# Optimization experiments

Measured on AMD Instinct MI355X. Metric: run time of the kernel, lower is better.

The kernel has to match this reference:

```python
import jax, jax.numpy as jnp
import numpy as np

B, T = 256, 512
E, H, V, C = 128, 256, 50000, 64


def setup_inputs() -> dict:
    key = jax.random.key(0)
    ks = jax.random.split(key, 8)
    k = 1.0 / np.sqrt(H)
    u = lambda kk, shape: jax.random.uniform(kk, shape, jnp.float32, -k, k)
    return {
        "sentence": jax.random.randint(ks[0], (B, T), 0, V),
        "emb": jax.random.normal(ks[1], (V, E), jnp.float32),
        "W_ih": u(ks[2], (4 * H, E)),
        "W_hh": u(ks[3], (4 * H, H)),
        "b_ih": u(ks[4], (4 * H,)),
        "b_hh": u(ks[5], (4 * H,)),
        "W_lin": u(ks[6], (C, H)),
        "b_lin": u(ks[7], (C,)),
    }


def reference(sentence, emb, W_ih, W_hh, b_ih, b_hh, W_lin, b_lin):
    x = emb[sentence]  # [B, T, E]
    # Precompute input-to-gate projections for all timesteps in one GEMM.
    x_proj = jnp.einsum('bte,ge->btg', x, W_ih) + b_ih + b_hh  # [B, T, 4H]

    def step(carry, xt):
        h, c = carry
        gates = xt + h @ W_hh.T  # [B, 4H], torch gate order i,f,g,o
        i, f, g, o = jnp.split(gates, 4, axis=-1)
        c = jax.nn.sigmoid(f) * c + jax.nn.sigmoid(i) * jnp.tanh(g)
        h = jax.nn.sigmoid(o) * jnp.tanh(c)
        return (h, c), h

    h0 = jnp.zeros((x.shape[0], W_hh.shape[1]), x.dtype)
    _, hs = jax.lax.scan(step, (h0, h0), jnp.swapaxes(x_proj, 0, 1))
    lstm_out = jnp.swapaxes(hs, 0, 1)  # [B, T, H]

    logits = lstm_out @ W_lin.T + b_lin  # [B, T, C]
    # Faithful to original: LogSoftmax over dim=1 (the TIME axis), then prod over time.
    all_probs = jax.nn.log_softmax(logits, axis=1)
    return jnp.prod(all_probs, axis=1)  # [B, C]
```

## Files before the change

kernel.cpp:

```cpp
#include <hip/hip_runtime.h>

#define TT 512
#define HH 256
#define EE 128
#define BB 256
#define CC 64
#define VV 50000
#define NSB 128

#define OFF_EMB   0ull
#define OFF_WHA   6400000ull
#define OFF_WXA   6662144ull
#define OFF_BIAS  6793216ull
#define OFF_WLIN  6797312ull
#define OFF_LSTM  6813696ull
#define OFF_LOG   73922560ull
#define WS_NEED   107476992ull

typedef __attribute__((ext_vector_type(4))) float    f32x4;
typedef __attribute__((ext_vector_type(4))) unsigned u32x4;
typedef __attribute__((ext_vector_type(4))) int      i32x4;
typedef __attribute__((ext_vector_type(8))) int      i32x8;
typedef __bf16 bf16x8_t __attribute__((ext_vector_type(8)));

__device__ __forceinline__ float rcp_f(float x) { return __builtin_amdgcn_rcpf(x); }
__device__ __forceinline__ float exp2_(float x) {
  float r; asm("v_exp_f32 %0, %1" : "=v"(r) : "v"(x)); return r;
}
__device__ __forceinline__ unsigned short to_bf16(float f) {
  unsigned u = __float_as_uint(f);
  return (unsigned short)((u + 0x7fffu + ((u >> 16) & 1u)) >> 16);
}
__device__ __forceinline__ unsigned enc4(float v) {
  const unsigned sg = (__float_as_uint(v) >> 31) << 3;
  const float a = fminf(fabsf(v), 6.0f);
  const float c = (a < 2.0f) ? __builtin_rintf(a + a)
                : (a < 4.0f) ? __builtin_rintf(a) + 2.0f
                             : __builtin_rintf(a * 0.5f) + 4.0f;
  return sg | (unsigned)(int)c;
}
__device__ __forceinline__ i32x8 up8(i32x4 v) {
  i32x8 r;
  r[0] = v[0]; r[1] = v[1]; r[2] = v[2]; r[3] = v[3];
  r[4] = 0; r[5] = 0; r[6] = 0; r[7] = 0;
  return r;
}
__device__ __forceinline__ f32x4 mfma4(i32x8 a, i32x8 b, f32x4 c, int sb) {
  return __builtin_amdgcn_mfma_scale_f32_16x16x128_f8f6f4(
      a, b, c, 4, 4, 0, 0x7f7f7f7f, 0, sb);
}
#define SB_H 0x7f7f7f7f
#define SB_X 0x80808080

#define LOG2E  1.442695041f
#define SN2    (-LOG2E / 256.f)
#define SG2    (-2.f * LOG2E / 256.f)
#define C2_    (-2.f * LOG2E)

__global__ void prep_emb(const float* __restrict__ emb, unsigned* __restrict__ out) {
  const int u = blockIdx.x * 256 + threadIdx.x;
  const f32x4 f0 = ((const f32x4*)emb)[u * 2];
  const f32x4 f1 = ((const f32x4*)emb)[u * 2 + 1];
  unsigned r = enc4(2.f * f0[0]) | (enc4(2.f * f0[1]) << 4);
  r |= (enc4(2.f * f0[2]) | (enc4(2.f * f0[3]) << 4)) << 8;
  r |= (enc4(2.f * f1[0]) | (enc4(2.f * f1[1]) << 4)) << 16;
  r |= (enc4(2.f * f1[2]) | (enc4(2.f * f1[3]) << 4)) << 24;
  out[u] = r;
}

__global__ void prep_wha(const float* __restrict__ Whh, unsigned char* __restrict__ wf) {
  const int id = blockIdx.x * 256 + threadIdx.x;
  const int byt = id & 15, l = (id >> 4) & 63;
  const int kt = (id >> 10) & 1, mt = (id >> 11) & 7, w8 = id >> 14;
  const int r16 = l & 15;
  const int grow = (r16 & 3) * 256 + w8 * 32 + mt * 4 + (r16 >> 2);
  const int k0 = kt * 128 + ((l >> 4) << 5) + byt * 2;
  const unsigned n0 = enc4(64.f * Whh[grow * HH + k0]);
  const unsigned n1 = enc4(64.f * Whh[grow * HH + k0 + 1]);
  wf[id] = (unsigned char)(n0 | (n1 << 4));
}

__global__ void prep_wxa(const float* __restrict__ Wih, unsigned char* __restrict__ wf) {
  const int id = blockIdx.x * 256 + threadIdx.x;
  const int byt = id & 15, l = (id >> 4) & 63;
  const int mt = (id >> 10) & 7, w8 = id >> 13;
  const int r16 = l & 15;
  const int grow = (r16 & 3) * 256 + w8 * 32 + mt * 4 + (r16 >> 2);
  const int k0 = ((l >> 4) << 5) + byt * 2;
  const unsigned n0 = enc4(64.f * Wih[grow * EE + k0]);
  const unsigned n1 = enc4(64.f * Wih[grow * EE + k0 + 1]);
  wf[id] = (unsigned char)(n0 | (n1 << 4));
}

__global__ void prep_bias(const float* __restrict__ bih, const float* __restrict__ bhh,
                          float* __restrict__ bp) {
  const int n = blockIdx.x * 256 + threadIdx.x;
  const float sc = (n >= 512 && n < 768) ? (-2.f * LOG2E) : (-LOG2E);
  bp[n] = (bih[n] + bhh[n]) * sc;
}

__global__ void prep_wlin(const float* __restrict__ Wlin, unsigned short* __restrict__ wl) {
  const int id = blockIdx.x * 256 + threadIdx.x;
  const int j = id & 7, l = (id >> 3) & 63;
  const int kk = (id >> 9) & 7, q = id >> 12;
  const int c = q * 16 + (l & 15);
  const int k = kk * 32 + ((l >> 4) << 3) + j;
  wl[id] = to_bf16(Wlin[c * HH + k]);
}

__global__ __launch_bounds__(1024, 1)
void lstm_scan(const int* __restrict__ sent, const unsigned char* __restrict__ emb4,
               const unsigned char* __restrict__ wha, const unsigned char* __restrict__ wxa,
               const float* __restrict__ bias, unsigned short* __restrict__ lstm_out) {
  __shared__ __align__(16) unsigned char xa[64 * 1024];
  __shared__ __align__(16) unsigned char bh[2 * 1024];
  __shared__ __align__(16) unsigned char xbuf[2][1024];
  __shared__ __align__(16) float redistf[16][272];
  __shared__ int sent_lds[4][512];

  const int tid = threadIdx.x;
  const int lane = tid & 63;
  const int w = tid >> 6;
  const int b0 = blockIdx.x << 2;

  i32x8 Ah[4][2];
#pragma unroll
  for (int m = 0; m < 4; ++m)
#pragma unroll
    for (int kt = 0; kt < 2; ++kt)
      Ah[m][kt] = up8(*(const i32x4*)(wha + (((w * 4 + m) * 2 + kt) * 64 + lane) * 16));

  for (int c = tid; c < 4096; c += 1024)
    ((u32x4*)xa)[c] = ((const u32x4*)wxa)[c];
  for (int i = tid; i < 2048; i += 1024)
    sent_lds[i >> 9][i & 511] = sent[(b0 + (i >> 9)) * TT + (i & 511)];
  if (tid < 512) ((int*)bh)[tid] = 0;

  const bool gth = (w < 8) && (lane < 8);
  const int gr = 2 * w + ((lane >> 2) & 1), gq = lane & 3;
  const int* sptr = &sent_lds[gr & 3][gr >> 2];
  const unsigned char* embg = emb4 + gq * 16;
  const int gwo = gq * 256 + gr * 16;

  __syncthreads();

  u32x4 xg;
  if (gth) {
    const int i0s = sptr[0];
    *(u32x4*)(xbuf[0] + gwo) = *(const u32x4*)(embg + (size_t)i0s * 64);
    const int i1s = sptr[4];
    *(u32x4*)(xbuf[1] + gwo) = *(const u32x4*)(embg + (size_t)i1s * 64);
    const int i2s = sptr[8];
    xg = *(const u32x4*)(embg + (size_t)i2s * 64);
  }
  __syncthreads();

  const int l16 = lane * 16;
  const f32x4 Zf = (f32x4){0.f, 0.f, 0.f, 0.f};
  f32x4 acc[4];
  {
    const i32x8 Bx = up8(*(const i32x4*)(xbuf[0] + l16));
#pragma unroll
    for (int m = 0; m < 4; ++m)
      acc[m] = mfma4(up8(*(const i32x4*)(xa + (w * 4 + m) * 1024 + l16)), Bx, Zf, SB_X);
  }

  const int s = lane & 3;
  const int hu = w * 16 + (lane >> 2);
  const int colJ = (lane & 15) >> 2;
  const float bi = bias[hu],       bf = bias[256 + hu],
              bg = bias[512 + hu], bo = bias[768 + hu];
  const int cb4 = (hu >> 7) * 1024 + ((hu & 127) >> 5) * 256 + s * 16 + ((hu & 31) >> 1);
  const int wroff = (lane >> 4) * 16 + s * 4;
  const int rdoff = (lane >> 4) * 68 + ((lane >> 2) & 3) * 16 + s * 4;
  const bool heven = ((lane >> 2) & 1) == 0;
  const long obase = ((long)(b0 + s) * TT) * HH + hu;
  float cs = 0.f;

#define MICRO(J) { \
  const i32x8 Bh0 = up8(*(const i32x4*)(bh + l16)); \
  const i32x8 Bh1 = up8(*(const i32x4*)(bh + 1024 + l16)); \
  __builtin_amdgcn_s_setprio(1); \
  _Pragma("unroll") for (int m = 0; m < 4; ++m) acc[m] = mfma4(Ah[m][0], Bh0, acc[m], SB_H); \
  _Pragma("unroll") for (int m = 0; m < 4; ++m) acc[m] = mfma4(Ah[m][1], Bh1, acc[m], SB_H); \
  __builtin_amdgcn_s_setprio(0); \
  if (colJ == (J)) { \
    _Pragma("unroll") for (int m = 0; m < 4; ++m) \
      *(f32x4*)&redistf[w][m * 68 + wroff] = acc[m]; \
  } \
  if ((J) == 2) { \
    if (dogS) *(u32x4*)(xbC + gwo) = xg; \
    if (dogL) { const int idx = sptr[(tb + 3) * 4]; \
                xg = *(const u32x4*)(embg + (size_t)idx * 64); } \
  } \
  if ((J) == 3) { \
    const i32x8 Bx = up8(*(const i32x4*)(xbN + l16)); \
    _Pragma("unroll") for (int m = 0; m < 4; ++m) \
      acc[m] = mfma4(up8(*(const i32x4*)(xa + (w * 4 + m) * 1024 + l16)), Bx, Zf, SB_X); \
  } \
  asm volatile("s_waitcnt lgkmcnt(0)" ::: "memory"); \
  __builtin_amdgcn_sched_barrier(0); \
  const f32x4 g = *(const f32x4*)&redistf[w][rdoff]; \
  const float si = rcp_f(1.f + exp2_(g[0] * SN2 + bi)); \
  const float sf = rcp_f(1.f + exp2_(g[1] * SN2 + bf)); \
  const float tg = 2.f * rcp_f(1.f + exp2_(g[2] * SG2 + bg)) - 1.f; \
  const float so = rcp_f(1.f + exp2_(g[3] * SN2 + bo)); \
  cs = sf * cs + si * tg; \
  const float tc = 2.f * rcp_f(1.f + exp2_(cs * C2_)) - 1.f; \
  const float hv = so * tc; \
  const float hvp = __shfl_xor(hv, 4); \
  if (heven) { \
    const unsigned nib = enc4(4.f * hv) | (enc4(4.f * hvp) << 4); \
    bh[cb4 + ((((J) + 1) & 3)) * 64] = (unsigned char)nib; \
    bh[cb4 + (J) * 64] = 0; \
    unsigned pb; asm("v_cvt_pk_bf16_f32 %0, %1, %2" : "=v"(pb) : "v"(hv), "v"(hvp)); \
    *(unsigned*)(lstm_out + obase + (long)(t0 + (J)) * HH) = pb; \
  } \
  asm volatile("s_waitcnt lgkmcnt(0)" ::: "memory"); \
  __builtin_amdgcn_s_barrier(); \
}

#pragma unroll 1
  for (int tb = 0; tb < NSB; ++tb) {
    const int t0 = tb << 2;
    const bool dogS = gth && (tb + 2 < NSB);
    const bool dogL = gth && (tb + 3 < NSB);
    unsigned char* xbC = xbuf[tb & 1];
    unsigned char* xbN = xbuf[(tb + 1) & 1];
    MICRO(0)
    MICRO(1)
    MICRO(2)
    MICRO(3)
  }
#undef MICRO
}

__global__ __launch_bounds__(256)
void logits_gemm(const unsigned short* __restrict__ lstm, const unsigned short* __restrict__ wl,
                 const float* __restrict__ blin, float* __restrict__ logits) {
  const int tid = threadIdx.x, l = tid & 63, wv = tid >> 6;
  const long m0 = (long)blockIdx.x * 64 + wv * 16;
  f32x4 ac[4];
#pragma unroll
  for (int q = 0; q < 4; ++q) ac[q] = (f32x4){0.f, 0.f, 0.f, 0.f};
  const unsigned short* arow = lstm + (m0 + (l & 15)) * HH + ((l >> 4) << 3);
#pragma unroll
  for (int kk = 0; kk < 8; ++kk) {
    const bf16x8_t a = __builtin_bit_cast(bf16x8_t, *(const u32x4*)(arow + kk * 32));
#pragma unroll
    for (int q = 0; q < 4; ++q) {
      const bf16x8_t b = __builtin_bit_cast(bf16x8_t, *(const u32x4*)(wl + (((q * 8 + kk) * 64 + l) << 3)));
      ac[q] = __builtin_amdgcn_mfma_f32_16x16x32_bf16(a, b, ac[q], 0, 0, 0);
    }
  }
  const int r0 = (l >> 4) << 2;
#pragma unroll
  for (int q = 0; q < 4; ++q) {
    const int col = q * 16 + (l & 15);
    const float bb = blin[col];
#pragma unroll
    for (int r = 0; r < 4; ++r)
      logits[(m0 + r0 + r) * CC + col] = ac[q][r] + bb;
  }
}

__global__ __launch_bounds__(256)
void softmax_prod(const float* __restrict__ logits, float* __restrict__ out) {
  __shared__ float lds[TT * CC];
  __shared__ float red[3][4][CC];
  const int tid = threadIdx.x, b = blockIdx.x;
  const f32x4* src = (const f32x4*)(logits + (long)b * TT * CC);
  f32x4* dst = (f32x4*)lds;
#pragma unroll 1
  for (int i = tid; i < TT * CC / 4; i += 256) dst[i] = src[i];
  __syncthreads();

  const int c = tid & 63, part = tid >> 6;
  const int t0 = part * 128;
  float m = -3.0e38f;
  for (int k = 0; k < 128; ++k) m = fmaxf(m, lds[(t0 + k) * CC + c]);
  red[0][part][c] = m;
  __syncthreads();
  m = fmaxf(fmaxf(red[0][0][c], red[0][1][c]), fmaxf(red[0][2][c], red[0][3][c]));

  float ssum = 0.f;
  for (int k = 0; k < 128; ++k) ssum += __expf(lds[(t0 + k) * CC + c] - m);
  red[1][part][c] = ssum;
  __syncthreads();
  ssum = red[1][0][c] + red[1][1][c] + red[1][2][c] + red[1][3][c];
  const float lse = m + __logf(ssum);

  float pacc = 0.f;
  for (int k = 0; k < 128; ++k) pacc += __log2f(fabsf(lds[(t0 + k) * CC + c] - lse));
  red[2][part][c] = pacc;
  __syncthreads();
  if (part == 0) {
    const float tot = red[2][0][c] + red[2][1][c] + red[2][2][c] + red[2][3][c];
    out[b * CC + c] = exp2f(fminf(tot, 127.0f));
  }
}

extern "C" void kernel_launch(void* const* d_in, const int* in_sizes, int n_in,
                              void* d_out, int out_size, void* d_ws, size_t ws_size,
                              hipStream_t stream) {
  (void)in_sizes; (void)n_in; (void)out_size;
  if (ws_size < WS_NEED) return;

  const int*   sent = (const int*)d_in[0];
  const float* emb  = (const float*)d_in[1];
  const float* Wih  = (const float*)d_in[2];
  const float* Whh  = (const float*)d_in[3];
  const float* bih  = (const float*)d_in[4];
  const float* bhh  = (const float*)d_in[5];
  const float* Wlin = (const float*)d_in[6];
  const float* blin = (const float*)d_in[7];
  float* out = (float*)d_out;
  char* ws = (char*)d_ws;

  unsigned char*  emb4 = (unsigned char*)(ws + OFF_EMB);
  unsigned char*  wha  = (unsigned char*)(ws + OFF_WHA);
  unsigned char*  wxa  = (unsigned char*)(ws + OFF_WXA);
  float*          bp   = (float*)(ws + OFF_BIAS);
  unsigned short* wl   = (unsigned short*)(ws + OFF_WLIN);
  unsigned short* lo   = (unsigned short*)(ws + OFF_LSTM);
  float*          lg   = (float*)(ws + OFF_LOG);

  prep_emb<<<3125, 256, 0, stream>>>(emb, (unsigned*)emb4);
  prep_wha<<<512, 256, 0, stream>>>(Whh, wha);
  prep_wxa<<<256, 256, 0, stream>>>(Wih, wxa);
  prep_bias<<<4, 256, 0, stream>>>(bih, bhh, bp);
  prep_wlin<<<64, 256, 0, stream>>>(Wlin, wl);
  lstm_scan<<<64, 1024, 0, stream>>>(sent, emb4, wha, wxa, bp, lo);
  logits_gemm<<<2048, 256, 0, stream>>>(lo, wl, blin, lg);
  softmax_prod<<<256, 256, 0, stream>>>(lg, out);
}
```

Baseline: 564.6 us.

## Split LSTM scan into 2-batch blocks of 8 waves with fused gate reciprocals

The recurrent scan kernel now gives each workgroup 2 batch rows instead of 4. It launches 128 blocks of 512 threads instead of 64 blocks of 1024, so more CUs take part in the serial scan. Each wave now owns 32 hidden units (8 MFMA tiles), and the time loop unrolls 8 steps per block iteration, with the redistribution and embedding-prefetch indexing remapped to match. The gate math also merges reciprocals: pairs of sigmoid and tanh denominators are multiplied together so each step needs 3 rcp instead of 6. This trades a shorter dependent chain and more parallel blocks for more register pressure per wave and a small risk of overflow in the combined denominators.

After: 514.7 us. 8.8% less time.

```diff
diff --git a/kernel.cpp b/kernel.cpp
--- a/kernel.cpp
+++ b/kernel.cpp
@@ -6,7 +6,7 @@
 #define BB 256
 #define CC 64
 #define VV 50000
-#define NSB 128
+#define NSB 64
 
 #define OFF_EMB   0ull
 #define OFF_WHA   6400000ull
@@ -108,37 +108,37 @@
   wl[id] = to_bf16(Wlin[c * HH + k]);
 }
 
-__global__ __launch_bounds__(1024, 1)
+__global__ __launch_bounds__(512, 1)
 void lstm_scan(const int* __restrict__ sent, const unsigned char* __restrict__ emb4,
                const unsigned char* __restrict__ wha, const unsigned char* __restrict__ wxa,
                const float* __restrict__ bias, unsigned short* __restrict__ lstm_out) {
   __shared__ __align__(16) unsigned char xa[64 * 1024];
   __shared__ __align__(16) unsigned char bh[2 * 1024];
   __shared__ __align__(16) unsigned char xbuf[2][1024];
-  __shared__ __align__(16) float redistf[16][272];
-  __shared__ int sent_lds[4][512];
+  __shared__ __align__(16) float redistf[8][544];
+  __shared__ int sent_lds[2][512];
 
   const int tid = threadIdx.x;
   const int lane = tid & 63;
   const int w = tid >> 6;
-  const int b0 = blockIdx.x << 2;
-
-  i32x8 Ah[4][2];
-#pragma unroll
-  for (int m = 0; m < 4; ++m)
+  const int b0 = blockIdx.x << 1;
+
+  i32x8 Ah[8][2];
+#pragma unroll
+  for (int mt = 0; mt < 8; ++mt)
 #pragma unroll
     for (int kt = 0; kt < 2; ++kt)
-      Ah[m][kt] = up8(*(const i32x4*)(wha + (((w * 4 + m) * 2 + kt) * 64 + lane) * 16));
-
-  for (int c = tid; c < 4096; c += 1024)
+      Ah[mt][kt] = up8(*(const i32x4*)(wha + (((w * 8 + mt) * 2 + kt) * 64 + lane) * 16));
+
+  for (int c = tid; c < 4096; c += 512)
     ((u32x4*)xa)[c] = ((const u32x4*)wxa)[c];
-  for (int i = tid; i < 2048; i += 1024)
+  for (int i = tid; i < 1024; i += 512)
     sent_lds[i >> 9][i & 511] = sent[(b0 + (i >> 9)) * TT + (i & 511)];
   if (tid < 512) ((int*)bh)[tid] = 0;
 
-  const bool gth = (w < 8) && (lane < 8);
+  const bool gth = lane < 8;
   const int gr = 2 * w + ((lane >> 2) & 1), gq = lane & 3;
-  const int* sptr = &sent_lds[gr & 3][gr >> 2];
+  const int* sptr = &sent_lds[gr & 1][gr >> 1];
   const unsigned char* embg = emb4 + gq * 16;
   const int gwo = gq * 256 + gr * 16;
 
@@ -148,32 +148,35 @@
   if (gth) {
     const int i0s = sptr[0];
     *(u32x4*)(xbuf[0] + gwo) = *(const u32x4*)(embg + (size_t)i0s * 64);
-    const int i1s = sptr[4];
+    const int i1s = sptr[8];
     *(u32x4*)(xbuf[1] + gwo) = *(const u32x4*)(embg + (size_t)i1s * 64);
-    const int i2s = sptr[8];
+    const int i2s = sptr[16];
     xg = *(const u32x4*)(embg + (size_t)i2s * 64);
   }
   __syncthreads();
 
   const int l16 = lane * 16;
   const f32x4 Zf = (f32x4){0.f, 0.f, 0.f, 0.f};
-  f32x4 acc[4];
+  f32x4 acc[8];
   {
     const i32x8 Bx = up8(*(const i32x4*)(xbuf[0] + l16));
 #pragma unroll
-    for (int m = 0; m < 4; ++m)
-      acc[m] = mfma4(up8(*(const i32x4*)(xa + (w * 4 + m) * 1024 + l16)), Bx, Zf, SB_X);
-  }
-
-  const int s = lane & 3;
-  const int hu = w * 16 + (lane >> 2);
-  const int colJ = (lane & 15) >> 2;
+    for (int mt = 0; mt < 8; ++mt)
+      acc[mt] = mfma4(up8(*(const i32x4*)(xa + ((w * 8 + mt) << 10) + l16)), Bx, Zf, SB_X);
+  }
+
+  const int s = lane & 1;
+  const int huL = lane >> 1;
+  const int hu = w * 32 + huL;
+  const int mtR = lane >> 3;
+  const int hulR = (lane >> 1) & 3;
   const float bi = bias[hu],       bf = bias[256 + hu],
               bg = bias[512 + hu], bo = bias[768 + hu];
-  const int cb4 = (hu >> 7) * 1024 + ((hu & 127) >> 5) * 256 + s * 16 + ((hu & 31) >> 1);
+  const int wc = (lane & 15) >> 1;
   const int wroff = (lane >> 4) * 16 + s * 4;
-  const int rdoff = (lane >> 4) * 68 + ((lane >> 2) & 3) * 16 + s * 4;
-  const bool heven = ((lane >> 2) & 1) == 0;
+  const int rdoff = mtR * 68 + hulR * 16 + s * 4;
+  const bool heven = (huL & 1) == 0;
+  const int cb4s = (hu >> 7) * 1024 + ((hu & 127) >> 5) * 256 + ((hu & 31) >> 1) + s * 16;
   const long obase = ((long)(b0 + s) * TT) * HH + hu;
   float cs = 0.f;
 
@@ -181,40 +184,43 @@
   const i32x8 Bh0 = up8(*(const i32x4*)(bh + l16)); \
   const i32x8 Bh1 = up8(*(const i32x4*)(bh + 1024 + l16)); \
   __builtin_amdgcn_s_setprio(1); \
-  _Pragma("unroll") for (int m = 0; m < 4; ++m) acc[m] = mfma4(Ah[m][0], Bh0, acc[m], SB_H); \
-  _Pragma("unroll") for (int m = 0; m < 4; ++m) acc[m] = mfma4(Ah[m][1], Bh1, acc[m], SB_H); \
+  _Pragma("unroll") for (int mt = 0; mt < 8; ++mt) acc[mt] = mfma4(Ah[mt][0], Bh0, acc[mt], SB_H); \
+  _Pragma("unroll") for (int mt = 0; mt < 8; ++mt) acc[mt] = mfma4(Ah[mt][1], Bh1, acc[mt], SB_H); \
   __builtin_amdgcn_s_setprio(0); \
-  if (colJ == (J)) { \
-    _Pragma("unroll") for (int m = 0; m < 4; ++m) \
-      *(f32x4*)&redistf[w][m * 68 + wroff] = acc[m]; \
+  if (wc == (J)) { \
+    _Pragma("unroll") for (int mt = 0; mt < 8; ++mt) \
+      *(f32x4*)&redistf[w][mt * 68 + wroff] = acc[mt]; \
   } \
-  if ((J) == 2) { \
+  if ((J) == 4) { \
     if (dogS) *(u32x4*)(xbC + gwo) = xg; \
-    if (dogL) { const int idx = sptr[(tb + 3) * 4]; \
+    if (dogL) { const int idx = sptr[(tb + 3) * 8]; \
                 xg = *(const u32x4*)(embg + (size_t)idx * 64); } \
   } \
-  if ((J) == 3) { \
+  if ((J) == 7) { \
     const i32x8 Bx = up8(*(const i32x4*)(xbN + l16)); \
-    _Pragma("unroll") for (int m = 0; m < 4; ++m) \
-      acc[m] = mfma4(up8(*(const i32x4*)(xa + (w * 4 + m) * 1024 + l16)), Bx, Zf, SB_X); \
+    _Pragma("unroll") for (int mt = 0; mt < 8; ++mt) \
+      acc[mt] = mfma4(up8(*(const i32x4*)(xa + ((w * 8 + mt) << 10) + l16)), Bx, Zf, SB_X); \
   } \
   asm volatile("s_waitcnt lgkmcnt(0)" ::: "memory"); \
   __builtin_amdgcn_sched_barrier(0); \
   const f32x4 g = *(const f32x4*)&redistf[w][rdoff]; \
-  const float si = rcp_f(1.f + exp2_(g[0] * SN2 + bi)); \
-  const float sf = rcp_f(1.f + exp2_(g[1] * SN2 + bf)); \
-  const float tg = 2.f * rcp_f(1.f + exp2_(g[2] * SG2 + bg)) - 1.f; \
-  const float so = rcp_f(1.f + exp2_(g[3] * SN2 + bo)); \
-  cs = sf * cs + si * tg; \
-  const float tc = 2.f * rcp_f(1.f + exp2_(cs * C2_)) - 1.f; \
-  const float hv = so * tc; \
-  const float hvp = __shfl_xor(hv, 4); \
+  const float ea = exp2_(g[0] * SN2 + bi); \
+  const float eb = exp2_(g[1] * SN2 + bf); \
+  const float ec = exp2_(g[2] * SG2 + bg); \
+  const float ed = exp2_(g[3] * SN2 + bo); \
+  const float r1 = rcp_f(1.f + eb); \
+  const float r2 = rcp_f((1.f + ea) * (1.f + ec)); \
+  cs = cs * r1 + (1.f - ec) * r2; \
+  const float ee = exp2_(cs * C2_); \
+  const float r3 = rcp_f((1.f + ee) * (1.f + ed)); \
+  const float hv = (1.f - ee) * r3; \
+  const float hvp = __shfl_xor(hv, 2); \
   if (heven) { \
     const unsigned nib = enc4(4.f * hv) | (enc4(4.f * hvp) << 4); \
-    bh[cb4 + ((((J) + 1) & 3)) * 64] = (unsigned char)nib; \
-    bh[cb4 + (J) * 64] = 0; \
+    bh[cb4s + ((((J) + 1) & 7)) * 32] = (unsigned char)nib; \
+    bh[cb4s + (J) * 32] = 0; \
     unsigned pb; asm("v_cvt_pk_bf16_f32 %0, %1, %2" : "=v"(pb) : "v"(hv), "v"(hvp)); \
-    *(unsigned*)(lstm_out + obase + (long)(t0 + (J)) * HH) = pb; \
+    *(unsigned*)(lstm_out + obase + (long)(tb * 8 + (J)) * HH) = pb; \
   } \
   asm volatile("s_waitcnt lgkmcnt(0)" ::: "memory"); \
   __builtin_amdgcn_s_barrier(); \
@@ -222,7 +228,6 @@
 
 #pragma unroll 1
   for (int tb = 0; tb < NSB; ++tb) {
-    const int t0 = tb << 2;
     const bool dogS = gth && (tb + 2 < NSB);
     const bool dogL = gth && (tb + 3 < NSB);
     unsigned char* xbC = xbuf[tb & 1];
@@ -231,6 +236,10 @@
     MICRO(1)
     MICRO(2)
     MICRO(3)
+    MICRO(4)
+    MICRO(5)
+    MICRO(6)
+    MICRO(7)
   }
 #undef MICRO
 }
@@ -330,7 +339,7 @@
   prep_wxa<<<256, 256, 0, stream>>>(Wih, wxa);
   prep_bias<<<4, 256, 0, stream>>>(bih, bhh, bp);
   prep_wlin<<<64, 256, 0, stream>>>(Wlin, wl);
-  lstm_scan<<<64, 1024, 0, stream>>>(sent, emb4, wha, wxa, bp, lo);
+  lstm_scan<<<128, 512, 0, stream>>>(sent, emb4, wha, wxa, bp, lo);
   logits_gemm<<<2048, 256, 0, stream>>>(lo, wl, blin, lg);
   softmax_prod<<<256, 256, 0, stream>>>(lg, out);
 }
```
